# Kernel tuning notes

Hardware: AMD Instinct MI355X
Metric: run time of the kernel (lower is better)

The kernel has to match this reference:

```python
import jax, jax.numpy as jnp
import numpy as np

NEG_SLOPE = 0.2  # PyG GATConv default leaky_relu slope


def _gat_layer(x, src, dst, n_nodes, W, a_src, a_dst, b, heads, out_ch):
    # x: [N, Fin] -> h: [N, H, C]
    h = (x @ W).reshape(n_nodes, heads, out_ch)
    alpha_s = jnp.einsum('nhc,hc->nh', h, a_src)  # [N, H]
    alpha_d = jnp.einsum('nhc,hc->nh', h, a_dst)  # [N, H]
    e = jax.nn.leaky_relu(alpha_s[src] + alpha_d[dst], NEG_SLOPE)  # [E, H]
    # segment softmax over edges grouped by destination node
    m = jax.ops.segment_max(e, dst, num_segments=n_nodes)          # [N, H]
    e = jnp.exp(e - m[dst])
    denom = jax.ops.segment_sum(e, dst, num_segments=n_nodes)      # [N, H]
    alpha = e / denom[dst]                                          # self-loops guarantee denom > 0
    msg = alpha[:, :, None] * h[src]                                # [E, H, C]
    out = jax.ops.segment_sum(msg, dst, num_segments=n_nodes)      # [N, H, C]
    return out.reshape(n_nodes, heads * out_ch) + b


def reference(x, edge_index, batch, W1, a_src1, a_dst1, b1, W2, a_src2, a_dst2, b2, fc_w, fc_b):
    n_nodes = x.shape[0]
    heads = a_src1.shape[0]
    # PyG GATConv adds self-loops by default
    loops = jnp.arange(n_nodes, dtype=edge_index.dtype)
    src = jnp.concatenate([edge_index[0], loops])
    dst = jnp.concatenate([edge_index[1], loops])

    h = _gat_layer(x, src, dst, n_nodes, W1, a_src1, a_dst1, b1, heads, 64)
    h = jax.nn.relu(h)  # dropout is identity in eval mode
    h = _gat_layer(h, src, dst, n_nodes, W2, a_src2, a_dst2, b2, heads, 16)
    h = jax.nn.relu(h)

    n_graphs = 64
    sums = jax.ops.segment_sum(h, batch, num_segments=n_graphs)                    # [G, 64]
    counts = jax.ops.segment_sum(jnp.ones((n_nodes,), h.dtype), batch, num_segments=n_graphs)
    pooled = sums / jnp.maximum(counts, 1.0)[:, None]                              # global_mean_pool
    return pooled @ fc_w + fc_b


def setup_inputs() -> dict:
    key = jax.random.key(0)
    ks = jax.random.split(key, 12)
    N, E, F_in, G = 50000, 800000, 128, 64
    H = 4
    x = jax.random.normal(ks[0], (N, F_in), jnp.float32)
    edge_index = jax.random.randint(ks[1], (2, E), 0, N, jnp.int32)
    batch = jnp.sort(jax.random.randint(ks[2], (N,), 0, G, jnp.int32))
    s1 = 1.0 / np.sqrt(F_in)
    s2 = 1.0 / np.sqrt(H * 64)
    s3 = 1.0 / np.sqrt(H * 16)
    return {
        'x': x,
        'edge_index': edge_index,
        'batch': batch,
        'W1': jax.random.normal(ks[3], (F_in, H * 64), jnp.float32) * s1,
        'a_src1': jax.random.normal(ks[4], (H, 64), jnp.float32) * s1,
        'a_dst1': jax.random.normal(ks[5], (H, 64), jnp.float32) * s1,
        'b1': jnp.zeros((H * 64,), jnp.float32),
        'W2': jax.random.normal(ks[6], (H * 64, H * 16), jnp.float32) * s2,
        'a_src2': jax.random.normal(ks[7], (H, 16), jnp.float32) * s2,
        'a_dst2': jax.random.normal(ks[8], (H, 16), jnp.float32) * s2,
        'b2': jnp.zeros((H * 16,), jnp.float32),
        'fc_w': jax.random.normal(ks[9], (H * 16, 32), jnp.float32) * s3,
        'fc_b': jnp.zeros((32,), jnp.float32),
    }
```

## Files before the change

kernel.cpp:

```cpp
#include <hip/hip_runtime.h>
#include <hip/hip_bf16.h>
#include <hip/hip_fp16.h>
#include <math.h>

#define HEADS 4
#define CAP 64

typedef _Float16 half8_t __attribute__((ext_vector_type(8)));
typedef float float4_t __attribute__((ext_vector_type(4)));


__global__ void init_cnt_k(int* cnt, unsigned short* slots, int N) {
    int i = blockIdx.x * blockDim.x + threadIdx.x;
    if (i < N) {
        cnt[i] = 1;
        slots[(size_t)i * CAP] = (unsigned short)i;
    }
}


__global__ void cvt_w1t_k(const float* __restrict__ W1, _Float16* __restrict__ BT) {
    int k = blockIdx.x;
    int n = threadIdx.x;
    BT[n * 128 + k] = (_Float16)W1[k * 256 + n];
}

__global__ void cvt_w2t_k(const float* __restrict__ W2, _Float16* __restrict__ BT) {
    int n = blockIdx.x;
    int k = threadIdx.x;
    BT[n * 256 + k] = (_Float16)W2[k * 64 + n];
}


__global__ __launch_bounds__(256) void fused_scatter_gemm1_k(
    const int* __restrict__ src, const int* __restrict__ dst,
    int* __restrict__ cnt, unsigned short* __restrict__ slots, int E, int SB,
    const float* __restrict__ A,
    const _Float16* __restrict__ BT,
    __half* __restrict__ hout,
    const float* __restrict__ avs,
    const float* __restrict__ avd,
    float* __restrict__ os,
    float* __restrict__ od, int M) {
    __shared__ _Float16 lds[4 * 16 * 72];

    if ((int)blockIdx.x < SB) {
        int T = SB * 256;
        int t0 = blockIdx.x * 256 + threadIdx.x;
        int d[8], s[8];
        #pragma unroll
        for (int k = 0; k < 8; k++) {
            int i = t0 + k * T;
            if (i < E) { d[k] = dst[i]; s[k] = src[i]; }
            else d[k] = -1;
        }
        int p[8];
        #pragma unroll
        for (int k = 0; k < 8; k++) {
            if (d[k] >= 0) p[k] = atomicAdd(&cnt[d[k]], 1);
        }
        #pragma unroll
        for (int k = 0; k < 8; k++) {
            if (d[k] >= 0 && p[k] < CAP)
                slots[(size_t)d[k] * CAP + p[k]] = (unsigned short)s[k];
        }
        return;
    }

    int bx = blockIdx.x - SB;
    int wave = threadIdx.x >> 6;
    int lane = threadIdx.x & 63;
    int q = lane >> 4;
    int c16 = lane & 15;
    int row0 = bx * 64 + wave * 16;

    half8_t a[4];
    int ar = row0 + c16;
    bool avalid = (ar < M);
    const float* ap = A + (size_t)ar * 128;
    #pragma unroll
    for (int ks = 0; ks < 4; ks++) {
        if (avalid) {
            float4 f0 = *(const float4*)(ap + ks * 32 + q * 8);
            float4 f1 = *(const float4*)(ap + ks * 32 + q * 8 + 4);
            half8_t h;
            h[0] = (_Float16)f0.x; h[1] = (_Float16)f0.y;
            h[2] = (_Float16)f0.z; h[3] = (_Float16)f0.w;
            h[4] = (_Float16)f1.x; h[5] = (_Float16)f1.y;
            h[6] = (_Float16)f1.z; h[7] = (_Float16)f1.w;
            a[ks] = h;
        } else {
            a[ks] = (half8_t)(_Float16)0.0f;
        }
    }

    float4_t acc[16];
    #pragma unroll
    for (int ct = 0; ct < 16; ct++) acc[ct] = (float4_t)0.f;

    #pragma unroll
    for (int ks = 0; ks < 4; ks++) {
        #pragma unroll
        for (int ct = 0; ct < 16; ct++) {
            half8_t b = *(const half8_t*)(BT + (size_t)(ct * 16 + c16) * 128 + ks * 32 + q * 8);
            acc[ct] = __builtin_amdgcn_mfma_f32_16x16x32_f16(a[ks], b, acc[ct], 0, 0, 0);
        }
    }

    float psh[4][4] = {}, pdh[4][4] = {};
    #pragma unroll
    for (int ct = 0; ct < 16; ct++) {
        int h = ct >> 2;
        int cih = (ct & 3) * 16 + c16;
        float as_v = avs[h * 64 + cih];
        float ad_v = avd[h * 64 + cih];
        #pragma unroll
        for (int r = 0; r < 4; r++) {
            psh[h][r] = fmaf(acc[ct][r], as_v, psh[h][r]);
            pdh[h][r] = fmaf(acc[ct][r], ad_v, pdh[h][r]);
        }
    }
    #pragma unroll
    for (int h = 0; h < 4; h++) {
        #pragma unroll
        for (int r = 0; r < 4; r++) {
            #pragma unroll
            for (int o = 8; o >= 1; o >>= 1) {
                psh[h][r] += __shfl_down(psh[h][r], o, 16);
                pdh[h][r] += __shfl_down(pdh[h][r], o, 16);
            }
        }
    }
    if (c16 == 0) {
        #pragma unroll
        for (int r = 0; r < 4; r++) {
            int gr = row0 + q * 4 + r;
            if (gr < M) {
                #pragma unroll
                for (int h = 0; h < 4; h++) {
                    os[(size_t)gr * HEADS + h] = psh[h][r];
                    od[(size_t)gr * HEADS + h] = pdh[h][r];
                }
            }
        }
    }

    _Float16* wl = lds + wave * (16 * 72);
    #pragma unroll
    for (int chunk = 0; chunk < 4; chunk++) {
        #pragma unroll
        for (int c4 = 0; c4 < 4; c4++) {
            int ct = chunk * 4 + c4;
            #pragma unroll
            for (int r = 0; r < 4; r++) {
                wl[(q * 4 + r) * 72 + c4 * 16 + c16] = (_Float16)acc[ct][r];
            }
        }
        __syncthreads();
        #pragma unroll
        for (int pass = 0; pass < 2; pass++) {
            int idx8 = pass * 64 + lane;
            int row = idx8 >> 3;
            int col8 = idx8 & 7;
            int gr = row0 + row;
            if (gr < M) {
                *(half8_t*)(hout + (size_t)gr * 256 + chunk * 64 + col8 * 8) =
                    *(const half8_t*)(wl + row * 72 + col8 * 8);
            }
        }
        __syncthreads();
    }
}


__global__ __launch_bounds__(256) void mfma_gemm2_k(
    const _Float16* __restrict__ Ah,
    const _Float16* __restrict__ BT,
    __half* __restrict__ hout,
    const float* __restrict__ avs,
    const float* __restrict__ avd,
    float* __restrict__ os,
    float* __restrict__ od, int M) {
    __shared__ _Float16 lds[4 * 16 * 64];
    int wave = threadIdx.x >> 6;
    int lane = threadIdx.x & 63;
    int q = lane >> 4;
    int c16 = lane & 15;
    int row0 = blockIdx.x * 64 + wave * 16;

    half8_t a[8];
    int ar = row0 + c16;
    bool avalid = (ar < M);
    const _Float16* ap = Ah + (size_t)ar * 256;
    #pragma unroll
    for (int ks = 0; ks < 8; ks++) {
        if (avalid) a[ks] = *(const half8_t*)(ap + ks * 32 + q * 8);
        else        a[ks] = (half8_t)(_Float16)0.0f;
    }

    float4_t acc[4];
    #pragma unroll
    for (int ct = 0; ct < 4; ct++) acc[ct] = (float4_t)0.f;

    #pragma unroll
    for (int ks = 0; ks < 8; ks++) {
        #pragma unroll
        for (int ct = 0; ct < 4; ct++) {
            half8_t b = *(const half8_t*)(BT + (size_t)(ct * 16 + c16) * 256 + ks * 32 + q * 8);
            acc[ct] = __builtin_amdgcn_mfma_f32_16x16x32_f16(a[ks], b, acc[ct], 0, 0, 0);
        }
    }

    float ps[4][4], pd[4][4];
    #pragma unroll
    for (int ct = 0; ct < 4; ct++) {
        float as_v = avs[ct * 16 + c16];
        float ad_v = avd[ct * 16 + c16];
        #pragma unroll
        for (int r = 0; r < 4; r++) {
            ps[ct][r] = acc[ct][r] * as_v;
            pd[ct][r] = acc[ct][r] * ad_v;
            #pragma unroll
            for (int o = 8; o >= 1; o >>= 1) {
                ps[ct][r] += __shfl_down(ps[ct][r], o, 16);
                pd[ct][r] += __shfl_down(pd[ct][r], o, 16);
            }
        }
    }
    if (c16 == 0) {
        #pragma unroll
        for (int r = 0; r < 4; r++) {
            int gr = row0 + q * 4 + r;
            if (gr < M) {
                #pragma unroll
                for (int ct = 0; ct < 4; ct++) {
                    os[(size_t)gr * HEADS + ct] = ps[ct][r];
                    od[(size_t)gr * HEADS + ct] = pd[ct][r];
                }
            }
        }
    }

    _Float16* wl = lds + wave * (16 * 64);
    #pragma unroll
    for (int ct = 0; ct < 4; ct++) {
        #pragma unroll
        for (int r = 0; r < 4; r++) {
            wl[(q * 4 + r) * 64 + ct * 16 + c16] = (_Float16)acc[ct][r];
        }
    }
    __syncthreads();
    #pragma unroll
    for (int pass = 0; pass < 2; pass++) {
        int idx8 = pass * 64 + lane;
        int row = idx8 >> 3;
        int col8 = idx8 & 7;
        int gr = row0 + row;
        if (gr < M) {
            *(half8_t*)(hout + (size_t)gr * 64 + col8 * 8) =
                *(const half8_t*)(wl + row * 64 + col8 * 8);
        }
    }
}


__global__ __launch_bounds__(256) void gat_agg64_f16_k(
    const __half* __restrict__ hsrc,
    const float* __restrict__ as,
    const float* __restrict__ ad,
    const int* __restrict__ cnt,
    const unsigned short* __restrict__ slots,
    const float* __restrict__ bias,
    __half* __restrict__ outh,
    int N) {
    int node = blockIdx.x * 4 + (threadIdx.x >> 6);
    if (node >= N) return;
    int l = threadIdx.x & 63;
    int h = l >> 4;
    int je = l & 15;
    int hb = h << 4;
    int deg = min(cnt[node], CAP);
    const unsigned short* sp = slots + (size_t)node * CAP;
    float adh = ad[(size_t)node * HEADS + h];
    float4 bv = *(const float4*)(bias + l * 4);
    float m = -INFINITY, den = 0.f;
    float4 acc = make_float4(0.f, 0.f, 0.f, 0.f);
    for (int base = 0; base < deg; base += 16) {
        int cl = min(16, deg - base);
        int s = 0;
        float e = -INFINITY;
        if (je < cl) {
            s = sp[base + je];
            float a = as[(size_t)s * HEADS + h] + adh;
            e = (a > 0.f) ? a : 0.2f * a;
        }
        float cmax = e;
        #pragma unroll
        for (int o = 8; o >= 1; o >>= 1) cmax = fmaxf(cmax, __shfl_xor(cmax, o));
        float m_new = fmaxf(m, cmax);
        float p = (je < cl) ? __expf(e - m_new) : 0.f;
        float sum = p;
        #pragma unroll
        for (int o = 8; o >= 1; o >>= 1) sum += __shfl_xor(sum, o);
        float sc = __expf(m - m_new);
        den = den * sc + sum;
        m = m_new;
        acc.x *= sc; acc.y *= sc; acc.z *= sc; acc.w *= sc;
        int j = 0;
        for (; j + 4 <= cl; j += 4) {
            float p0 = __shfl(p, hb + j),     p1 = __shfl(p, hb + j + 1);
            float p2 = __shfl(p, hb + j + 2), p3 = __shfl(p, hb + j + 3);
            int s0 = __shfl(s, hb + j),     s1 = __shfl(s, hb + j + 1);
            int s2 = __shfl(s, hb + j + 2), s3 = __shfl(s, hb + j + 3);
            uint2 r0 = *(const uint2*)(hsrc + (size_t)s0 * 256 + l * 4);
            uint2 r1 = *(const uint2*)(hsrc + (size_t)s1 * 256 + l * 4);
            uint2 r2 = *(const uint2*)(hsrc + (size_t)s2 * 256 + l * 4);
            uint2 r3 = *(const uint2*)(hsrc + (size_t)s3 * 256 + l * 4);
            float2 a0 = __half22float2(*(__half2*)&r0.x), b0 = __half22float2(*(__half2*)&r0.y);
            float2 a1 = __half22float2(*(__half2*)&r1.x), b1 = __half22float2(*(__half2*)&r1.y);
            float2 a2 = __half22float2(*(__half2*)&r2.x), b2 = __half22float2(*(__half2*)&r2.y);
            float2 a3 = __half22float2(*(__half2*)&r3.x), b3 = __half22float2(*(__half2*)&r3.y);
            acc.x = fmaf(p0, a0.x, acc.x); acc.y = fmaf(p0, a0.y, acc.y);
            acc.z = fmaf(p0, b0.x, acc.z); acc.w = fmaf(p0, b0.y, acc.w);
            acc.x = fmaf(p1, a1.x, acc.x); acc.y = fmaf(p1, a1.y, acc.y);
            acc.z = fmaf(p1, b1.x, acc.z); acc.w = fmaf(p1, b1.y, acc.w);
            acc.x = fmaf(p2, a2.x, acc.x); acc.y = fmaf(p2, a2.y, acc.y);
            acc.z = fmaf(p2, b2.x, acc.z); acc.w = fmaf(p2, b2.y, acc.w);
            acc.x = fmaf(p3, a3.x, acc.x); acc.y = fmaf(p3, a3.y, acc.y);
            acc.z = fmaf(p3, b3.x, acc.z); acc.w = fmaf(p3, b3.y, acc.w);
        }
        for (; j < cl; j++) {
            float pj = __shfl(p, hb + j);
            int sj = __shfl(s, hb + j);
            uint2 r0 = *(const uint2*)(hsrc + (size_t)sj * 256 + l * 4);
            float2 a0 = __half22float2(*(__half2*)&r0.x), b0 = __half22float2(*(__half2*)&r0.y);
            acc.x = fmaf(pj, a0.x, acc.x); acc.y = fmaf(pj, a0.y, acc.y);
            acc.z = fmaf(pj, b0.x, acc.z); acc.w = fmaf(pj, b0.y, acc.w);
        }
    }
    float inv = 1.f / den;
    float rx = fmaxf(fmaf(acc.x, inv, bv.x), 0.f);
    float ry = fmaxf(fmaf(acc.y, inv, bv.y), 0.f);
    float rz = fmaxf(fmaf(acc.z, inv, bv.z), 0.f);
    float rw = fmaxf(fmaf(acc.w, inv, bv.w), 0.f);
    __half2* op = (__half2*)(outh + (size_t)node * 256 + l * 4);
    op[0] = __floats2half2_rn(rx, ry);
    op[1] = __floats2half2_rn(rz, rw);
}


__global__ __launch_bounds__(256) void gat_agg16_f16_k(
    const __half* __restrict__ hsrc,
    const float* __restrict__ as,
    const float* __restrict__ ad,
    const int* __restrict__ cnt,
    const unsigned short* __restrict__ slots,
    const float* __restrict__ bias,
    float* __restrict__ out, int N) {
    int node = blockIdx.x * 4 + (threadIdx.x >> 6);
    if (node >= N) return;
    int l = threadIdx.x & 63;
    int ha = l >> 4;
    int je = l & 15;
    int q = l & 15;
    int hh = q >> 2;
    int eg = l >> 4;
    int deg = min(cnt[node], CAP);
    const unsigned short* sp = slots + (size_t)node * CAP;
    float adh = ad[(size_t)node * HEADS + ha];
    float m = -INFINITY, den = 0.f;
    float4 acc = make_float4(0.f, 0.f, 0.f, 0.f);
    for (int base = 0; base < deg; base += 16) {
        int cl = min(16, deg - base);
        int s = 0;
        float e = -INFINITY;
        if (je < cl) {
            s = sp[base + je];
            float a = as[(size_t)s * HEADS + ha] + adh;
            e = (a > 0.f) ? a : 0.2f * a;
        }
        float cmax = e;
        #pragma unroll
        for (int o = 8; o >= 1; o >>= 1) cmax = fmaxf(cmax, __shfl_xor(cmax, o));
        float m_new = fmaxf(m, cmax);
        float p = (je < cl) ? __expf(e - m_new) : 0.f;
        float sum = p;
        #pragma unroll
        for (int o = 8; o >= 1; o >>= 1) sum += __shfl_xor(sum, o);
        float sc = __expf(m - m_new);
        den = den * sc + sum;
        m = m_new;
        float sch = __shfl(sc, hh << 4);
        acc.x *= sch; acc.y *= sch; acc.z *= sch; acc.w *= sch;
        for (int j0 = 0; j0 < cl; j0 += 4) {
            int j = j0 + eg;
            int jc = min(j, cl - 1);
            float pj = __shfl(p, (hh << 4) + jc);
            int sj = __shfl(s, (hh << 4) + jc);
            if (j < cl) {
                uint2 raw = *(const uint2*)(hsrc + (size_t)sj * 64 + q * 4);
                float2 f0 = __half22float2(*(__half2*)&raw.x);
                float2 f1 = __half22float2(*(__half2*)&raw.y);
                acc.x = fmaf(pj, f0.x, acc.x); acc.y = fmaf(pj, f0.y, acc.y);
                acc.z = fmaf(pj, f1.x, acc.z); acc.w = fmaf(pj, f1.y, acc.w);
            }
        }
    }
    acc.x += __shfl_xor(acc.x, 16); acc.y += __shfl_xor(acc.y, 16);
    acc.z += __shfl_xor(acc.z, 16); acc.w += __shfl_xor(acc.w, 16);
    acc.x += __shfl_xor(acc.x, 32); acc.y += __shfl_xor(acc.y, 32);
    acc.z += __shfl_xor(acc.z, 32); acc.w += __shfl_xor(acc.w, 32);
    float denh = __shfl(den, hh << 4);
    if (eg == 0) {
        float inv = 1.f / denh;
        float4 bv = *(const float4*)(bias + q * 4);
        float4 r;
        r.x = fmaxf(fmaf(acc.x, inv, bv.x), 0.f);
        r.y = fmaxf(fmaf(acc.y, inv, bv.y), 0.f);
        r.z = fmaxf(fmaf(acc.z, inv, bv.z), 0.f);
        r.w = fmaxf(fmaf(acc.w, inv, bv.w), 0.f);
        *(float4*)(out + (size_t)node * 64 + q * 4) = r;
    }
}


__global__ void graph_bounds_k(const int* __restrict__ batch, int N, int* __restrict__ bstart) {
    int g = threadIdx.x;
    if (g <= 64) {
        int lo = 0, hi = N;
        while (lo < hi) {
            int mid = (lo + hi) >> 1;
            if (batch[mid] < g) lo = mid + 1; else hi = mid;
        }
        bstart[g] = lo;
    }
}

__global__ void pool_zero_k(float* __restrict__ sums) {
    sums[blockIdx.x * blockDim.x + threadIdx.x] = 0.f;
}

__global__ __launch_bounds__(256) void pool_sum_k(const float* __restrict__ g2,
                                                  const int* __restrict__ batch,
                                                  float* __restrict__ sums, int N) {
    int c = threadIdx.x & 63;
    int r = threadIdx.x >> 6;
    int base = blockIdx.x * 256;
    int lim = min(base + 256, N);
    float acc = 0.f;
    int cur = -1;
    for (int n = base + r; n < lim; n += 4) {
        int g = batch[n];
        if (g != cur) {
            if (cur >= 0) atomicAdd(&sums[cur * 64 + c], acc);
            acc = 0.f;
            cur = g;
        }
        acc += g2[(size_t)n * 64 + c];
    }
    if (cur >= 0) atomicAdd(&sums[cur * 64 + c], acc);
}

__global__ void fc_k(const float* __restrict__ sums, const int* __restrict__ bstart,
                     const float* __restrict__ w, const float* __restrict__ b,
                     float* __restrict__ out) {
    int g = blockIdx.x, o = threadIdx.x;
    float cnt_ = (float)max(bstart[g + 1] - bstart[g], 1);
    float inv = 1.f / cnt_;
    float acc = b[o];
    for (int k = 0; k < 64; k++) acc = fmaf(sums[g * 64 + k] * inv, w[k * 32 + o], acc);
    out[g * 32 + o] = acc;
}


static inline size_t align_up(size_t x, size_t a) { return (x + a - 1) & ~(a - 1); }

extern "C" void kernel_launch(void* const* d_in, const int* in_sizes, int n_in,
                              void* d_out, int out_size, void* d_ws, size_t ws_size,
                              hipStream_t stream) {
    const float* x      = (const float*)d_in[0];
    const int*   ei     = (const int*)d_in[1];
    const int*   batch  = (const int*)d_in[2];
    const float* W1     = (const float*)d_in[3];
    const float* a_src1 = (const float*)d_in[4];
    const float* a_dst1 = (const float*)d_in[5];
    const float* b1     = (const float*)d_in[6];
    const float* W2     = (const float*)d_in[7];
    const float* a_src2 = (const float*)d_in[8];
    const float* a_dst2 = (const float*)d_in[9];
    const float* b2     = (const float*)d_in[10];
    const float* fc_w   = (const float*)d_in[11];
    const float* fc_b   = (const float*)d_in[12];
    float* out = (float*)d_out;

    const int N = in_sizes[2];
    const int E = in_sizes[1] / 2;
    const int F_in = in_sizes[0] / N;
    const int D1 = HEADS * 64;
    const int D2 = HEADS * 16;

    const int* src = ei;
    const int* dst = ei + E;

    char* w = (char*)d_ws;
    size_t off = 0;
    auto alloc = [&](size_t bytes) {
        size_t p = off;
        off = align_up(off + bytes, 256);
        return (void*)(w + p);
    };
    int* cnt    = (int*)alloc((size_t)N * 4);
    unsigned short* slots = (unsigned short*)alloc((size_t)N * CAP * 2);
    int* bstart = (int*)alloc(65 * 4);
    float* pooled = (float*)alloc(64 * 64 * 4);
    float* as1  = (float*)alloc((size_t)N * HEADS * 4);
    float* ad1  = (float*)alloc((size_t)N * HEADS * 4);
    float* as2  = (float*)alloc((size_t)N * HEADS * 4);
    float* ad2  = (float*)alloc((size_t)N * HEADS * 4);
    __half* h1h = (__half*)alloc((size_t)N * D1 * 2);
    __half* g1h = (__half*)alloc((size_t)N * D1 * 2);
    __half* h2h = (__half*)alloc((size_t)N * D2 * 2);
    float* g2   = (float*)alloc((size_t)N * D2 * 4);
    _Float16* w1t = (_Float16*)alloc((size_t)F_in * D1 * 2);
    _Float16* w2t = (_Float16*)alloc((size_t)D1 * D2 * 2);

    init_cnt_k<<<(N + 255) / 256, 256, 0, stream>>>(cnt, slots, N);
    cvt_w1t_k<<<F_in, D1, 0, stream>>>(W1, w1t);
    cvt_w2t_k<<<D2, D1, 0, stream>>>(W2, w2t);

    const int SB = (E + 2047) / 2048;
    const int GB = (N + 63) / 64;
    fused_scatter_gemm1_k<<<SB + GB, 256, 0, stream>>>(
        src, dst, cnt, slots, E, SB,
        x, w1t, h1h, a_src1, a_dst1, as1, ad1, N);

    gat_agg64_f16_k<<<(N + 3) / 4, 256, 0, stream>>>(h1h, as1, ad1, cnt, slots, b1, g1h, N);

    mfma_gemm2_k<<<(N + 63) / 64, 256, 0, stream>>>((const _Float16*)g1h, w2t, h2h,
                                                    a_src2, a_dst2, as2, ad2, N);
    gat_agg16_f16_k<<<(N + 3) / 4, 256, 0, stream>>>(h2h, as2, ad2, cnt, slots, b2, g2, N);

    graph_bounds_k<<<1, 128, 0, stream>>>(batch, N, bstart);
    pool_zero_k<<<16, 256, 0, stream>>>(pooled);
    pool_sum_k<<<(N + 255) / 256, 256, 0, stream>>>(g2, batch, pooled, N);
    fc_k<<<64, 32, 0, stream>>>(pooled, bstart, fc_w, fc_b, out);
}
```

Measured before the change: 320.2 us.

## Fuse layer-2 GEMM into layer-1 aggregation using fdot2 per node

Removes the separate MFMA GEMM2 kernel and the g1h intermediate buffer. Each wave now stages its aggregated 256-wide fp16 row in LDS and computes the 64 outputs of h1·W2 directly with packed fp16 dot2 instructions against a pair-packed W2. It also computes the layer-2 attention logits in the same pass. This avoids a 25.6MB write plus read of g1 and one launch. In exchange it does scalar dot-product work per node instead of tensor-core matmul, and every wave re-reads W2 from cache.

New measurement: 324.8 us. No clear change (+1.4%).

```diff
diff --git a/kernel.cpp b/kernel.cpp
--- a/kernel.cpp
+++ b/kernel.cpp
@@ -7,7 +7,20 @@
 #define CAP 64
 
 typedef _Float16 half8_t __attribute__((ext_vector_type(8)));
+typedef _Float16 half2v __attribute__((ext_vector_type(2)));
 typedef float float4_t __attribute__((ext_vector_type(4)));
+
+__device__ __forceinline__ float dot2f16(unsigned a, unsigned b, float c) {
+#if __has_builtin(__builtin_amdgcn_fdot2)
+    union U { unsigned u; half2v h; };
+    U ua, ub; ua.u = a; ub.u = b;
+    return __builtin_amdgcn_fdot2(ua.h, ub.h, c, false);
+#else
+    __half2 ha = *(__half2*)&a, hb = *(__half2*)&b;
+    float2 fa = __half22float2(ha), fb = __half22float2(hb);
+    return fmaf(fa.x, fb.x, fmaf(fa.y, fb.y, c));
+#endif
+}
 
 
 __global__ void init_cnt_k(int* cnt, unsigned short* slots, int N) {
@@ -25,10 +38,11 @@
     BT[n * 128 + k] = (_Float16)W1[k * 256 + n];
 }
 
-__global__ void cvt_w2t_k(const float* __restrict__ W2, _Float16* __restrict__ BT) {
-    int n = blockIdx.x;
-    int k = threadIdx.x;
-    BT[n * 256 + k] = (_Float16)W2[k * 64 + n];
+__global__ void cvt_w2p_k(const float* __restrict__ W2, unsigned* __restrict__ P) {
+    int c2 = blockIdx.x;
+    int n = threadIdx.x;
+    __half2 h = __floats2half2_rn(W2[(2 * c2) * 64 + n], W2[(2 * c2 + 1) * 64 + n]);
+    P[c2 * 64 + n] = *(unsigned*)&h;
 }
 
 
@@ -173,107 +187,23 @@
 }
 
 
-__global__ __launch_bounds__(256) void mfma_gemm2_k(
-    const _Float16* __restrict__ Ah,
-    const _Float16* __restrict__ BT,
-    __half* __restrict__ hout,
-    const float* __restrict__ avs,
-    const float* __restrict__ avd,
-    float* __restrict__ os,
-    float* __restrict__ od, int M) {
-    __shared__ _Float16 lds[4 * 16 * 64];
-    int wave = threadIdx.x >> 6;
-    int lane = threadIdx.x & 63;
-    int q = lane >> 4;
-    int c16 = lane & 15;
-    int row0 = blockIdx.x * 64 + wave * 16;
-
-    half8_t a[8];
-    int ar = row0 + c16;
-    bool avalid = (ar < M);
-    const _Float16* ap = Ah + (size_t)ar * 256;
-    #pragma unroll
-    for (int ks = 0; ks < 8; ks++) {
-        if (avalid) a[ks] = *(const half8_t*)(ap + ks * 32 + q * 8);
-        else        a[ks] = (half8_t)(_Float16)0.0f;
-    }
-
-    float4_t acc[4];
-    #pragma unroll
-    for (int ct = 0; ct < 4; ct++) acc[ct] = (float4_t)0.f;
-
-    #pragma unroll
-    for (int ks = 0; ks < 8; ks++) {
-        #pragma unroll
-        for (int ct = 0; ct < 4; ct++) {
-            half8_t b = *(const half8_t*)(BT + (size_t)(ct * 16 + c16) * 256 + ks * 32 + q * 8);
-            acc[ct] = __builtin_amdgcn_mfma_f32_16x16x32_f16(a[ks], b, acc[ct], 0, 0, 0);
-        }
-    }
-
-    float ps[4][4], pd[4][4];
-    #pragma unroll
-    for (int ct = 0; ct < 4; ct++) {
-        float as_v = avs[ct * 16 + c16];
-        float ad_v = avd[ct * 16 + c16];
-        #pragma unroll
-        for (int r = 0; r < 4; r++) {
-            ps[ct][r] = acc[ct][r] * as_v;
-            pd[ct][r] = acc[ct][r] * ad_v;
-            #pragma unroll
-            for (int o = 8; o >= 1; o >>= 1) {
-                ps[ct][r] += __shfl_down(ps[ct][r], o, 16);
-                pd[ct][r] += __shfl_down(pd[ct][r], o, 16);
-            }
-        }
-    }
-    if (c16 == 0) {
-        #pragma unroll
-        for (int r = 0; r < 4; r++) {
-            int gr = row0 + q * 4 + r;
-            if (gr < M) {
-                #pragma unroll
-                for (int ct = 0; ct < 4; ct++) {
-                    os[(size_t)gr * HEADS + ct] = ps[ct][r];
-                    od[(size_t)gr * HEADS + ct] = pd[ct][r];
-                }
-            }
-        }
-    }
-
-    _Float16* wl = lds + wave * (16 * 64);
-    #pragma unroll
-    for (int ct = 0; ct < 4; ct++) {
-        #pragma unroll
-        for (int r = 0; r < 4; r++) {
-            wl[(q * 4 + r) * 64 + ct * 16 + c16] = (_Float16)acc[ct][r];
-        }
-    }
-    __syncthreads();
-    #pragma unroll
-    for (int pass = 0; pass < 2; pass++) {
-        int idx8 = pass * 64 + lane;
-        int row = idx8 >> 3;
-        int col8 = idx8 & 7;
-        int gr = row0 + row;
-        if (gr < M) {
-            *(half8_t*)(hout + (size_t)gr * 64 + col8 * 8) =
-                *(const half8_t*)(wl + row * 64 + col8 * 8);
-        }
-    }
-}
-
-
-__global__ __launch_bounds__(256) void gat_agg64_f16_k(
+__global__ __launch_bounds__(256) void gat_agg64_gemm2_k(
     const __half* __restrict__ hsrc,
     const float* __restrict__ as,
     const float* __restrict__ ad,
     const int* __restrict__ cnt,
     const unsigned short* __restrict__ slots,
     const float* __restrict__ bias,
-    __half* __restrict__ outh,
+    const unsigned* __restrict__ w2p,
+    const float* __restrict__ avs2,
+    const float* __restrict__ avd2,
+    __half* __restrict__ h2out,
+    float* __restrict__ os2,
+    float* __restrict__ od2,
     int N) {
-    int node = blockIdx.x * 4 + (threadIdx.x >> 6);
+    __shared__ unsigned g1buf[4][128];
+    int wv = threadIdx.x >> 6;
+    int node = blockIdx.x * 4 + wv;
     if (node >= N) return;
     int l = threadIdx.x & 63;
     int h = l >> 4;
@@ -343,9 +273,39 @@
     float ry = fmaxf(fmaf(acc.y, inv, bv.y), 0.f);
     float rz = fmaxf(fmaf(acc.z, inv, bv.z), 0.f);
     float rw = fmaxf(fmaf(acc.w, inv, bv.w), 0.f);
-    __half2* op = (__half2*)(outh + (size_t)node * 256 + l * 4);
-    op[0] = __floats2half2_rn(rx, ry);
-    op[1] = __floats2half2_rn(rz, rw);
+
+    __half2 h01 = __floats2half2_rn(rx, ry);
+    __half2 h23 = __floats2half2_rn(rz, rw);
+    g1buf[wv][l * 2 + 0] = *(unsigned*)&h01;
+    g1buf[wv][l * 2 + 1] = *(unsigned*)&h23;
+    float h2v = 0.f;
+    const unsigned* wp = w2p + l;
+    #pragma unroll 4
+    for (int c4 = 0; c4 < 32; c4++) {
+        uint4 g4 = *(const uint4*)&g1buf[wv][c4 * 4];
+        unsigned w0 = wp[(c4 * 4 + 0) * 64];
+        unsigned w1 = wp[(c4 * 4 + 1) * 64];
+        unsigned w2v = wp[(c4 * 4 + 2) * 64];
+        unsigned w3 = wp[(c4 * 4 + 3) * 64];
+        h2v = dot2f16(g4.x, w0, h2v);
+        h2v = dot2f16(g4.y, w1, h2v);
+        h2v = dot2f16(g4.z, w2v, h2v);
+        h2v = dot2f16(g4.w, w3, h2v);
+    }
+
+    float asv = avs2[(l >> 4) * 16 + (l & 15)];
+    float adv = avd2[(l >> 4) * 16 + (l & 15)];
+    float ps = h2v * asv, pd = h2v * adv;
+    #pragma unroll
+    for (int o = 8; o >= 1; o >>= 1) {
+        ps += __shfl_down(ps, o, 16);
+        pd += __shfl_down(pd, o, 16);
+    }
+    if ((l & 15) == 0) {
+        os2[(size_t)node * HEADS + (l >> 4)] = ps;
+        od2[(size_t)node * HEADS + (l >> 4)] = pd;
+    }
+    h2out[(size_t)node * 64 + l] = __float2half(h2v);
 }
 
 
@@ -518,15 +478,14 @@
     float* as2  = (float*)alloc((size_t)N * HEADS * 4);
     float* ad2  = (float*)alloc((size_t)N * HEADS * 4);
     __half* h1h = (__half*)alloc((size_t)N * D1 * 2);
-    __half* g1h = (__half*)alloc((size_t)N * D1 * 2);
     __half* h2h = (__half*)alloc((size_t)N * D2 * 2);
     float* g2   = (float*)alloc((size_t)N * D2 * 4);
     _Float16* w1t = (_Float16*)alloc((size_t)F_in * D1 * 2);
-    _Float16* w2t = (_Float16*)alloc((size_t)D1 * D2 * 2);
+    unsigned* w2p = (unsigned*)alloc((size_t)128 * 64 * 4);
 
     init_cnt_k<<<(N + 255) / 256, 256, 0, stream>>>(cnt, slots, N);
     cvt_w1t_k<<<F_in, D1, 0, stream>>>(W1, w1t);
-    cvt_w2t_k<<<D2, D1, 0, stream>>>(W2, w2t);
+    cvt_w2p_k<<<128, 64, 0, stream>>>(W2, w2p);
 
     const int SB = (E + 2047) / 2048;
     const int GB = (N + 63) / 64;
@@ -534,10 +493,9 @@
         src, dst, cnt, slots, E, SB,
         x, w1t, h1h, a_src1, a_dst1, as1, ad1, N);
 
-    gat_agg64_f16_k<<<(N + 3) / 4, 256, 0, stream>>>(h1h, as1, ad1, cnt, slots, b1, g1h, N);
-
-    mfma_gemm2_k<<<(N + 63) / 64, 256, 0, stream>>>((const _Float16*)g1h, w2t, h2h,
-                                                    a_src2, a_dst2, as2, ad2, N);
+    gat_agg64_gemm2_k<<<(N + 3) / 4, 256, 0, stream>>>(
+        h1h, as1, ad1, cnt, slots, b1, w2p, a_src2, a_dst2, h2h, as2, ad2, N);
+
     gat_agg16_f16_k<<<(N + 3) / 4, 256, 0, stream>>>(h2h, as2, ad2, cnt, slots, b2, g2, N);
 
     graph_bounds_k<<<1, 128, 0, stream>>>(batch, N, bstart);
```
